# Optimization experiments

Hardware: AMD Instinct MI355X
Metric: run time of the kernel (lower is better)

Reference implementation:

```python
import jax, jax.numpy as jnp
import numpy as np

B, H, L, C = 16, 512, 4096, 1
LAM = 0.001  # kernel squash threshold (lam in LongConvKernel)


def setup_inputs() -> dict:
    key = jax.random.key(0)
    ks = jax.random.split(key, 5)
    u = jax.random.normal(ks[0], (B, H, L), jnp.float32)
    # LongConvKernel 'double_exp' init: K ~ N(0, 0.02^2) * exp(-(j/L) * (H//2)^(i/H))
    K = jax.random.normal(ks[1], (C, H, L), jnp.float32) * 0.02
    i = jnp.arange(H, dtype=jnp.float32)[:, None]
    j = jnp.arange(L, dtype=jnp.float32)[None, :]
    double_exp = jnp.exp(-(j / L) * jnp.power(float(H // 2), i / H))  # (H, L)
    kernel = K * double_exp[None]
    D = jax.random.normal(ks[2], (C, H), jnp.float32)  # skip connection params
    # TransposedLinear(C*H -> H): weight (d_output, d_input), kaiming-ish scale
    Wout = jax.random.normal(ks[3], (H, C * H), jnp.float32) / np.sqrt(C * H)
    bout = jax.random.normal(ks[4], (H,), jnp.float32) * 0.01
    return {"u": u, "kernel": kernel, "D": D, "Wout": Wout, "bout": bout}


def reference(u, kernel, D, Wout, bout):
    Lseq = u.shape[-1]
    # kernel squashing: relu(|k| - lam) * sign(k)  (soft-threshold)
    k = jax.nn.relu(jnp.abs(kernel) - LAM) * jnp.sign(kernel)  # (C, H, L)
    n = 2 * Lseq
    k_f = jnp.fft.rfft(k, n=n, axis=-1)            # (C, H, n//2+1) complex
    u_f = jnp.fft.rfft(u, n=n, axis=-1)            # (B, H, n//2+1) complex
    y_f = jnp.einsum('bhl,chl->bchl', u_f, k_f)    # pointwise multiply in freq
    y = jnp.fft.irfft(y_f, n=n, axis=-1)[..., :Lseq]  # (B, C, H, L)
    y = y + jnp.einsum('bhl,ch->bchl', u, D)       # skip term
    y = y.reshape(y.shape[0], C * H, Lseq)         # (B, C*H, L)
    y = jax.nn.gelu(y, approximate=False)          # activation (torch GELU = exact)
    # output_linear: TransposedLinear + swish postact
    y = jnp.einsum('bul,vu->bvl', y, Wout) + bout[None, :, None]
    y = jax.nn.silu(y)
    return y
```

## Files before the change

### kernel.cpp

```cpp
#include <hip/hip_runtime.h>
#include <hip/hip_bf16.h>
#include <math.h>

#define BB 16
#define HH 512
#define LL 4096
#define NFFT 8192
#define LAM 0.001f

typedef __attribute__((ext_vector_type(8))) short short8;
typedef __attribute__((ext_vector_type(4))) float floatx4;

#define R2C 0.70710678118654752f

__device__ __forceinline__ void cmul(float ar, float ai, float br, float bi,
                                     float& cr, float& ci) {
  cr = ar * br - ai * bi;
  ci = ar * bi + ai * br;
}

constexpr float W16C[8] = {1.f, 0.92387953f, 0.70710678f, 0.38268343f, 0.f,
                           -0.38268343f, -0.70710678f, -0.92387953f};
constexpr float W16S[8] = {0.f, -0.38268343f, -0.70710678f, -0.92387953f, -1.f,
                           -0.92387953f, -0.70710678f, -0.38268343f};
constexpr int BR8[8] = {0, 4, 2, 6, 1, 5, 3, 7};
constexpr float W16CB[8] = {W16C[0], W16C[4], W16C[2], W16C[6],
                            W16C[1], W16C[5], W16C[3], W16C[7]};
constexpr float W16SB[8] = {W16S[0], W16S[4], W16S[2], W16S[6],
                            W16S[1], W16S[5], W16S[3], W16S[7]};

__device__ __forceinline__ int slotf(int a) { return a ^ ((a >> 4) & 15); }

__device__ __forceinline__ void fft8(float* r, float* i) {
  float t0r = r[0] + r[4], t0i = i[0] + i[4], u0r = r[0] - r[4], u0i = i[0] - i[4];
  float t1r = r[1] + r[5], t1i = i[1] + i[5], u1r = r[1] - r[5], u1i = i[1] - i[5];
  float t2r = r[2] + r[6], t2i = i[2] + i[6], u2r = r[2] - r[6], u2i = i[2] - i[6];
  float t3r = r[3] + r[7], t3i = i[3] + i[7], u3r = r[3] - r[7], u3i = i[3] - i[7];
  float w1r = R2C * (u1r + u1i), w1i = R2C * (u1i - u1r);
  float w2r = u2i, w2i = -u2r;
  float w3r = R2C * (u3i - u3r), w3i = -R2C * (u3r + u3i);
  float p0r = t0r + t2r, p0i = t0i + t2i, q0r = t0r - t2r, q0i = t0i - t2i;
  float p1r = t1r + t3r, p1i = t1i + t3i, q1r = t1r - t3r, q1i = t1i - t3i;
  float s1r = q1i, s1i = -q1r;
  float v0r = u0r + w2r, v0i = u0i + w2i, x0r = u0r - w2r, x0i = u0i - w2i;
  float v1r = w1r + w3r, v1i = w1i + w3i, x1r = w1r - w3r, x1i = w1i - w3i;
  float y1r = x1i, y1i = -x1r;
  r[0] = p0r + p1r; i[0] = p0i + p1i;
  r[1] = p0r - p1r; i[1] = p0i - p1i;
  r[2] = q0r + s1r; i[2] = q0i + s1i;
  r[3] = q0r - s1r; i[3] = q0i - s1i;
  r[4] = v0r + v1r; i[4] = v0i + v1i;
  r[5] = v0r - v1r; i[5] = v0i - v1i;
  r[6] = x0r + y1r; i[6] = x0i + y1i;
  r[7] = x0r - y1r; i[7] = x0i - y1i;
}

__device__ __forceinline__ void fft8_pad4(float* r, float* i) {
  float x0r = r[0], x0i = i[0], x1r = r[1], x1i = i[1];
  float x2r = r[2], x2i = i[2], x3r = r[3], x3i = i[3];
  float w1r = R2C * (x1r + x1i), w1i = R2C * (x1i - x1r);
  float w2r = x2i, w2i = -x2r;
  float w3r = R2C * (x3i - x3r), w3i = -R2C * (x3r + x3i);
  float p0r = x0r + x2r, p0i = x0i + x2i, q0r = x0r - x2r, q0i = x0i - x2i;
  float p1r = x1r + x3r, p1i = x1i + x3i, q1r = x1r - x3r, q1i = x1i - x3i;
  float s1r = q1i, s1i = -q1r;
  float v0r = x0r + w2r, v0i = x0i + w2i, m0r = x0r - w2r, m0i = x0i - w2i;
  float v1r = w1r + w3r, v1i = w1i + w3i, m1r = w1r - w3r, m1i = w1i - w3i;
  float y1r = m1i, y1i = -m1r;
  r[0] = p0r + p1r; i[0] = p0i + p1i;
  r[1] = p0r - p1r; i[1] = p0i - p1i;
  r[2] = q0r + s1r; i[2] = q0i + s1i;
  r[3] = q0r - s1r; i[3] = q0i - s1i;
  r[4] = v0r + v1r; i[4] = v0i + v1i;
  r[5] = v0r - v1r; i[5] = v0i - v1i;
  r[6] = m0r + y1r; i[6] = m0i + y1i;
  r[7] = m0r - y1r; i[7] = m0i - y1i;
}

__device__ __forceinline__ void ifft8(float* r, float* i) {
  float p0r = r[0] + r[1], p0i = i[0] + i[1];
  float p1r = r[0] - r[1], p1i = i[0] - i[1];
  float q0r = r[2] + r[3], q0i = i[2] + i[3];
  float s1r = r[2] - r[3], s1i = i[2] - i[3];
  float v0r = r[4] + r[5], v0i = i[4] + i[5];
  float v1r = r[4] - r[5], v1i = i[4] - i[5];
  float x0r = r[6] + r[7], x0i = i[6] + i[7];
  float y1r = r[6] - r[7], y1i = i[6] - i[7];
  float q1r = -s1i, q1i = s1r;
  float x1r = -y1i, x1i = y1r;
  float t0r = p0r + q0r, t0i = p0i + q0i, t2r = p0r - q0r, t2i = p0i - q0i;
  float t1r = p1r + q1r, t1i = p1i + q1i, t3r = p1r - q1r, t3i = p1i - q1i;
  float a0r = v0r + x0r, a0i = v0i + x0i, a2r = v0r - x0r, a2i = v0i - x0i;
  float a1r = v1r + x1r, a1i = v1i + x1i, a3r = v1r - x1r, a3i = v1i - x1i;
  float u1r = R2C * (a1r - a1i), u1i = R2C * (a1r + a1i);
  float u2r = -a2i, u2i = a2r;
  float u3r = -R2C * (a3r + a3i), u3i = R2C * (a3r - a3i);
  r[0] = t0r + a0r; i[0] = t0i + a0i;  r[4] = t0r - a0r; i[4] = t0i - a0i;
  r[1] = t1r + u1r; i[1] = t1i + u1i;  r[5] = t1r - u1r; i[5] = t1i - u1i;
  r[2] = t2r + u2r; i[2] = t2i + u2i;  r[6] = t2r - u2r; i[6] = t2i - u2i;
  r[3] = t3r + u3r; i[3] = t3i + u3i;  r[7] = t3r - u3r; i[7] = t3i - u3i;
}

__device__ __forceinline__ void ifft8_head4(float* r, float* i) {
  float p0r = r[0] + r[1], p0i = i[0] + i[1];
  float p1r = r[0] - r[1], p1i = i[0] - i[1];
  float q0r = r[2] + r[3], q0i = i[2] + i[3];
  float s1r = r[2] - r[3], s1i = i[2] - i[3];
  float v0r = r[4] + r[5], v0i = i[4] + i[5];
  float v1r = r[4] - r[5], v1i = i[4] - i[5];
  float x0r = r[6] + r[7], x0i = i[6] + i[7];
  float y1r = r[6] - r[7], y1i = i[6] - i[7];
  float q1r = -s1i, q1i = s1r;
  float x1r = -y1i, x1i = y1r;
  float t0r = p0r + q0r, t0i = p0i + q0i, t2r = p0r - q0r, t2i = p0i - q0i;
  float t1r = p1r + q1r, t1i = p1i + q1i, t3r = p1r - q1r, t3i = p1i - q1i;
  float a0r = v0r + x0r, a0i = v0i + x0i, a2r = v0r - x0r, a2i = v0i - x0i;
  float a1r = v1r + x1r, a1i = v1i + x1i, a3r = v1r - x1r, a3i = v1i - x1i;
  float u1r = R2C * (a1r - a1i), u1i = R2C * (a1r + a1i);
  float u2r = -a2i, u2i = a2r;
  float u3r = -R2C * (a3r + a3i), u3i = R2C * (a3r - a3i);
  r[0] = t0r + a0r; i[0] = t0i + a0i;
  r[1] = t1r + u1r; i[1] = t1i + u1i;
  r[2] = t2r + u2r; i[2] = t2i + u2i;
  r[3] = t3r + u3r; i[3] = t3i + u3i;
}

__device__ __forceinline__ float gelu_exact(float y) {
  return 0.5f * y * (1.f + erff(y * 0.70710678118654752f));
}

template <int LOGJ>
__device__ __forceinline__ void r8_fwd(float2* sb, int t, const float4* tw) {
  const int J = 1 << LOGJ;
  const int j = t & (J - 1);
  const int base = (t >> LOGJ) << (LOGJ + 3);
  float xr[8], xi[8];
#pragma unroll
  for (int s = 0; s < 8; ++s) {
    float2 v = sb[slotf(base + j + (s << LOGJ))];
    xr[s] = v.x; xi[s] = v.y;
  }
  fft8(xr, xi);
#pragma unroll
  for (int q = 0; q < 4; ++q) {
    float4 w = tw[(q << LOGJ) + j];
    float tr, ti;
    cmul(xr[2 * q], xi[2 * q], w.x, w.y, tr, ti);
    sb[slotf(base + (BR8[2 * q] << LOGJ) + j)] = make_float2(tr, ti);
    cmul(xr[2 * q + 1], xi[2 * q + 1], w.z, w.w, tr, ti);
    sb[slotf(base + (BR8[2 * q + 1] << LOGJ) + j)] = make_float2(tr, ti);
  }
}

template <int LOGJ>
__device__ __forceinline__ void r8_inv(float2* sb, int t, const float4* tw) {
  const int J = 1 << LOGJ;
  const int j = t & (J - 1);
  const int base = (t >> LOGJ) << (LOGJ + 3);
  float xr[8], xi[8];
#pragma unroll
  for (int q = 0; q < 4; ++q) {
    float4 w = tw[(q << LOGJ) + j];
    float2 v0 = sb[slotf(base + (BR8[2 * q] << LOGJ) + j)];
    cmul(v0.x, v0.y, w.x, -w.y, xr[2 * q], xi[2 * q]);
    float2 v1 = sb[slotf(base + (BR8[2 * q + 1] << LOGJ) + j)];
    cmul(v1.x, v1.y, w.z, -w.w, xr[2 * q + 1], xi[2 * q + 1]);
  }
  ifft8(xr, xi);
#pragma unroll
  for (int s = 0; s < 8; ++s)
    sb[slotf(base + j + (s << LOGJ))] = make_float2(xr[s], xi[s]);
}

__device__ __forceinline__ void p1_scatter(float2* sb, int j, const float4* tw1,
                                           float* xr, float* xi) {
#pragma unroll
  for (int q = 0; q < 4; ++q) {
    float4 w = tw1[(q << 10) + j];
    float tr, ti;
    cmul(xr[2 * q], xi[2 * q], w.x, w.y, tr, ti);
    sb[slotf((BR8[2 * q] << 10) + j)] = make_float2(tr, ti);
    cmul(xr[2 * q + 1], xi[2 * q + 1], w.z, w.w, tr, ti);
    sb[slotf((BR8[2 * q + 1] << 10) + j)] = make_float2(tr, ti);
  }
}

__device__ __forceinline__ void p4_bins(float2* sb, int t, float* br_, float* bi_) {
  const int p = t >> 1, par = t & 1;
  const int a0 = (p << 4) + par;
  float xr[8], xi[8];
#pragma unroll
  for (int e = 0; e < 8; ++e) {
    float2 v = sb[slotf(a0 + 2 * e)];
    xr[e] = v.x; xi[e] = v.y;
  }
  fft8(xr, xi);
#pragma unroll
  for (int s = 0; s < 8; ++s) {
    float tr, ti;
    if (par) { cmul(xr[s], xi[s], W16CB[s], W16SB[s], tr, ti); }
    else { tr = xr[s]; ti = xi[s]; }
    float orr = __shfl_xor(tr, 1);
    float oii = __shfl_xor(ti, 1);
    br_[s] = par ? (orr - tr) : (tr + orr);
    bi_[s] = par ? (oii - ti) : (ti + oii);
  }
}

__device__ __forceinline__ void p4_inv(float2* sb, int t, float* br_, float* bi_) {
  const int p = t >> 1, par = t & 1;
  const int a0 = (p << 4) + par;
  float yr[8], yi[8];
#pragma unroll
  for (int s = 0; s < 8; ++s) {
    float orr = __shfl_xor(br_[s], 1);
    float oii = __shfl_xor(bi_[s], 1);
    float er = par ? (orr - br_[s]) : (br_[s] + orr);
    float ei = par ? (oii - bi_[s]) : (bi_[s] + oii);
    if (par) { float tr, ti; cmul(er, ei, W16CB[s], -W16SB[s], tr, ti); er = tr; ei = ti; }
    yr[s] = er; yi[s] = ei;
  }
  ifft8(yr, yi);
#pragma unroll
  for (int e = 0; e < 8; ++e)
    sb[slotf(a0 + 2 * e)] = make_float2(yr[e], yi[e]);
}

__global__ __launch_bounds__(1024) void twgen_kernel(float4* __restrict__ tw1,
                                                     float4* __restrict__ tw2,
                                                     float4* __restrict__ tw3) {
  const int j = threadIdx.x;
#pragma unroll
  for (int q = 0; q < 4; ++q) {
    const int m0 = BR8[2 * q], m1 = BR8[2 * q + 1];
    float s0, c0, s1, c1;
    const float a1 = -6.283185307179586f / 8192.f;
    sincosf(a1 * (float)(j * m0), &s0, &c0);
    sincosf(a1 * (float)(j * m1), &s1, &c1);
    tw1[(q << 10) + j] = make_float4(c0, s0, c1, s1);
    if (j < 128) {
      const float a2 = -6.283185307179586f / 1024.f;
      sincosf(a2 * (float)(j * m0), &s0, &c0);
      sincosf(a2 * (float)(j * m1), &s1, &c1);
      tw2[(q << 7) + j] = make_float4(c0, s0, c1, s1);
    }
    if (j < 16) {
      const float a3 = -6.283185307179586f / 128.f;
      sincosf(a3 * (float)(j * m0), &s0, &c0);
      sincosf(a3 * (float)(j * m1), &s1, &c1);
      tw3[(q << 4) + j] = make_float4(c0, s0, c1, s1);
    }
  }
}

__global__ void wconv_kernel(const float* __restrict__ W,
                             __hip_bfloat16* __restrict__ Wb) {
  int i = blockIdx.x * 256 + threadIdx.x;
  Wb[i] = __float2bfloat16(W[i]);
}

__global__ __launch_bounds__(1024)
void kf_kernel(const float* __restrict__ kern, const float* __restrict__ D,
               float* __restrict__ Kf, const float4* __restrict__ tw1,
               const float4* __restrict__ tw2, const float4* __restrict__ tw3) {
  __shared__ __align__(16) float2 sb[NFFT];
  __shared__ __align__(16) float4 ltw2[512];
  __shared__ __align__(16) float4 ltw3[64];
  const int t = threadIdx.x;
  const int h = blockIdx.x;
  const float* kr = kern + (size_t)h * LL;
  if (t < 512) ltw2[t] = tw2[t];
  if (t < 64) ltw3[t] = tw3[t];
  {
    float xr[8], xi[8];
#pragma unroll
    for (int s = 0; s < 4; ++s) {
      float kv = kr[t + (s << 10)];
      float a = fabsf(kv) - LAM;
      float sq = (a > 0.f) ? ((kv > 0.f) ? a : -a) : 0.f;
      xr[s] = sq * (1.f / 8192.f);
      xi[s] = 0.f;
    }
    fft8_pad4(xr, xi);
    p1_scatter(sb, t, tw1, xr, xi);
  }
  __syncthreads();
  r8_fwd<7>(sb, t, ltw2);
  __syncthreads();
  r8_fwd<4>(sb, t, ltw3);
  {
    float br_[8], bi_[8];
    p4_bins(sb, t, br_, bi_);
    const float dsc = D[h] * (1.f / 8192.f);
    float4* out4 = (float4*)(Kf + (size_t)h * NFFT * 2) + (t << 2);
#pragma unroll
    for (int q = 0; q < 4; ++q)
      out4[q] = make_float4(br_[2 * q] + dsc, bi_[2 * q],
                            br_[2 * q + 1] + dsc, bi_[2 * q + 1]);
  }
}

__global__ __launch_bounds__(1024)
void fftconv_kernel(const float* __restrict__ u, const float* __restrict__ Kf,
                    __hip_bfloat16* __restrict__ g, const float4* __restrict__ tw1,
                    const float4* __restrict__ tw2, const float4* __restrict__ tw3) {
  __shared__ __align__(16) float2 sb[NFFT];
  __shared__ __align__(16) float4 ltw2[512];
  __shared__ __align__(16) float4 ltw3[64];
  const int t = threadIdx.x;
  const int h = blockIdx.x;
  const int p = blockIdx.y;
  const int b0 = 2 * p, b1 = 2 * p + 1;
  const float* u0 = u + ((size_t)(b0 * HH + h)) * LL;
  const float* u1 = u + ((size_t)(b1 * HH + h)) * LL;

  if (t < 512) ltw2[t] = tw2[t];
  if (t < 64) ltw3[t] = tw3[t];

  {
    float xr[8], xi[8];
#pragma unroll
    for (int s = 0; s < 4; ++s) {
      xr[s] = u0[t + (s << 10)];
      xi[s] = u1[t + (s << 10)];
    }
    fft8_pad4(xr, xi);
    p1_scatter(sb, t, tw1, xr, xi);
  }
  __syncthreads();
  r8_fwd<7>(sb, t, ltw2);
  __syncthreads();
  r8_fwd<4>(sb, t, ltw3);
  {
    float br_[8], bi_[8];
    p4_bins(sb, t, br_, bi_);
    const float4* kf4 = (const float4*)(Kf + (size_t)h * NFFT * 2) + (t << 2);
#pragma unroll
    for (int q = 0; q < 4; ++q) {
      float4 kk = kf4[q];
      float tr, ti;
      cmul(br_[2 * q], bi_[2 * q], kk.x, kk.y, tr, ti);
      br_[2 * q] = tr; bi_[2 * q] = ti;
      cmul(br_[2 * q + 1], bi_[2 * q + 1], kk.z, kk.w, tr, ti);
      br_[2 * q + 1] = tr; bi_[2 * q + 1] = ti;
    }
    p4_inv(sb, t, br_, bi_);
  }
  r8_inv<4>(sb, t, ltw3);
  __syncthreads();
  r8_inv<7>(sb, t, ltw2);
  __syncthreads();
  {
    float xr[8], xi[8];
#pragma unroll
    for (int q = 0; q < 4; ++q) {
      float4 w = tw1[(q << 10) + t];
      float2 v0 = sb[slotf((BR8[2 * q] << 10) + t)];
      cmul(v0.x, v0.y, w.x, -w.y, xr[2 * q], xi[2 * q]);
      float2 v1 = sb[slotf((BR8[2 * q + 1] << 10) + t)];
      cmul(v1.x, v1.y, w.z, -w.w, xr[2 * q + 1], xi[2 * q + 1]);
    }
    ifft8_head4(xr, xi);
    __hip_bfloat16* g0 = g + ((size_t)(b0 * HH + h)) * LL;
    __hip_bfloat16* g1 = g + ((size_t)(b1 * HH + h)) * LL;
#pragma unroll
    for (int s = 0; s < 4; ++s) {
      g0[t + (s << 10)] = __float2bfloat16(gelu_exact(xr[s]));
      g1[t + (s << 10)] = __float2bfloat16(gelu_exact(xi[s]));
    }
  }
}

__global__ __launch_bounds__(256) void transpose_kernel(
    const __hip_bfloat16* __restrict__ g, __hip_bfloat16* __restrict__ g2) {
  __shared__ unsigned short tile[64][72];
  const int lb = blockIdx.x;
  const int hb = blockIdx.y;
  const int b = blockIdx.z;
  const int l0 = lb * 64, h0 = hb * 64;
  const int tid = threadIdx.x;
  const int r = tid >> 3;
  const int gc = tid & 7;
  const int c = gc * 8;
  const unsigned short* gs = (const unsigned short*)g;
  unsigned short* g2s = (unsigned short*)g2;
  for (int it = 0; it < 2; ++it) {
    int rr = r + it * 32;
    int4 v = *(const int4*)(gs + ((size_t)(b * HH + h0 + rr)) * LL + l0 + c);
    *(int4*)&tile[rr][(gc ^ (rr >> 3)) << 3] = v;
  }
  __syncthreads();
  for (int it = 0; it < 2; ++it) {
    int rr = r + it * 32;
    const int pc = (rr & 7) | (((rr >> 3) ^ gc) << 3);
    unsigned short vals[8];
#pragma unroll
    for (int j = 0; j < 8; ++j) vals[j] = tile[c + j][pc];
    *(int4*)(g2s + ((size_t)(b * LL + l0 + rr)) * HH + h0 + c) = *(int4*)vals;
  }
}

__global__ __launch_bounds__(256, 4) void gemm_kernel(
    const __hip_bfloat16* __restrict__ Wb, const __hip_bfloat16* __restrict__ g2,
    const float* __restrict__ bout, float* __restrict__ out) {
  const int vt = blockIdx.x;
  const int lt = blockIdx.y;
  const int b = blockIdx.z;
  const int wave = threadIdx.x >> 6;
  const int ln = threadIdx.x & 63;
  const int wr = wave >> 1, wc = wave & 1;
  const int vbase = vt * 128 + wr * 64;
  const int lbase = lt * 128 + wc * 64;
  const int lane16 = ln & 15;
  const int quad = ln >> 4;

  floatx4 acc[4][4];
#pragma unroll
  for (int mi = 0; mi < 4; ++mi)
#pragma unroll
    for (int ni = 0; ni < 4; ++ni) acc[mi][ni] = (floatx4){0.f, 0.f, 0.f, 0.f};

  const unsigned short* A = (const unsigned short*)Wb;
  const unsigned short* Bm = (const unsigned short*)g2 + (size_t)b * LL * HH;

  for (int k0 = 0; k0 < HH; k0 += 32) {
    const int kk = k0 + quad * 8;
    short8 af[4], bf[4];
#pragma unroll
    for (int mi = 0; mi < 4; ++mi) {
      const int m = vbase + mi * 16 + lane16;
      af[mi] = *(const short8*)(A + (size_t)m * HH + kk);
    }
#pragma unroll
    for (int ni = 0; ni < 4; ++ni) {
      const int n = lbase + ni * 16 + lane16;
      bf[ni] = *(const short8*)(Bm + (size_t)n * HH + kk);
    }
#pragma unroll
    for (int mi = 0; mi < 4; ++mi)
#pragma unroll
      for (int ni = 0; ni < 4; ++ni)
        acc[mi][ni] = __builtin_amdgcn_mfma_f32_16x16x32_bf16(af[mi], bf[ni],
                                                              acc[mi][ni], 0, 0, 0);
  }

#pragma unroll
  for (int mi = 0; mi < 4; ++mi) {
#pragma unroll
    for (int r = 0; r < 4; ++r) {
      const int m = vbase + mi * 16 + quad * 4 + r;
      const float bias = bout[m];
#pragma unroll
      for (int ni = 0; ni < 4; ++ni) {
        const int n = lbase + ni * 16 + lane16;
        float y = acc[mi][ni][r] + bias;
        y = y / (1.f + __expf(-y));
        out[((size_t)(b * HH + m)) * LL + n] = y;
      }
    }
  }
}

extern "C" void kernel_launch(void* const* d_in, const int* in_sizes, int n_in,
                              void* d_out, int out_size, void* d_ws, size_t ws_size,
                              hipStream_t stream) {
  const float* u = (const float*)d_in[0];
  const float* kern = (const float*)d_in[1];
  const float* D = (const float*)d_in[2];
  const float* Wout = (const float*)d_in[3];
  const float* bout = (const float*)d_in[4];
  float* out = (float*)d_out;

  char* ws = (char*)d_ws;
  const size_t KF_BYTES = (size_t)HH * NFFT * sizeof(float2);
  const size_t G_BYTES = (size_t)BB * HH * LL * 2;
  float* Kf = (float*)ws;
  __hip_bfloat16* g = (__hip_bfloat16*)(ws + KF_BYTES);
  __hip_bfloat16* g2 = (__hip_bfloat16*)(ws + KF_BYTES + G_BYTES);
  __hip_bfloat16* Wb = (__hip_bfloat16*)(ws + KF_BYTES + 2 * G_BYTES);
  float4* tw1 = (float4*)g2;
  float4* tw2 = tw1 + 4 * 1024;
  float4* tw3 = tw2 + 4 * 128;

  twgen_kernel<<<dim3(1), dim3(1024), 0, stream>>>(tw1, tw2, tw3);
  wconv_kernel<<<dim3((HH * HH) / 256), dim3(256), 0, stream>>>(Wout, Wb);
  kf_kernel<<<dim3(HH), dim3(1024), 0, stream>>>(kern, D, Kf, tw1, tw2, tw3);
  fftconv_kernel<<<dim3(HH, BB / 2), dim3(1024), 0, stream>>>(u, Kf, g, tw1, tw2, tw3);
  transpose_kernel<<<dim3(LL / 64, HH / 64, BB), dim3(256), 0, stream>>>(g, g2);
  gemm_kernel<<<dim3(HH / 128, LL / 128, BB), dim3(256), 0, stream>>>(Wb, g2, bout, out);
}
```

Baseline: 537.8 us.

## Fuse transpose into GEMM via double-buffered LDS staging of activations

```diff
diff --git a/kernel.cpp b/kernel.cpp
--- a/kernel.cpp
+++ b/kernel.cpp
@@ -371,46 +371,22 @@
   }
 }
 
-__global__ __launch_bounds__(256) void transpose_kernel(
-    const __hip_bfloat16* __restrict__ g, __hip_bfloat16* __restrict__ g2) {
-  __shared__ unsigned short tile[64][72];
-  const int lb = blockIdx.x;
-  const int hb = blockIdx.y;
-  const int b = blockIdx.z;
-  const int l0 = lb * 64, h0 = hb * 64;
+#define BKP 40
+__global__ __launch_bounds__(256, 4) void gemm_kernel(
+    const __hip_bfloat16* __restrict__ Wb, const __hip_bfloat16* __restrict__ g,
+    const float* __restrict__ bout, float* __restrict__ out) {
+  __shared__ unsigned short bt[2][128][BKP];
+  const int id = blockIdx.x;
+  const int w = (id & 7) * 256 + (id >> 3);
+  const int vt = w & 3;
+  const int lt = (w >> 2) & 31;
+  const int b = w >> 7;
   const int tid = threadIdx.x;
-  const int r = tid >> 3;
-  const int gc = tid & 7;
-  const int c = gc * 8;
-  const unsigned short* gs = (const unsigned short*)g;
-  unsigned short* g2s = (unsigned short*)g2;
-  for (int it = 0; it < 2; ++it) {
-    int rr = r + it * 32;
-    int4 v = *(const int4*)(gs + ((size_t)(b * HH + h0 + rr)) * LL + l0 + c);
-    *(int4*)&tile[rr][(gc ^ (rr >> 3)) << 3] = v;
-  }
-  __syncthreads();
-  for (int it = 0; it < 2; ++it) {
-    int rr = r + it * 32;
-    const int pc = (rr & 7) | (((rr >> 3) ^ gc) << 3);
-    unsigned short vals[8];
-#pragma unroll
-    for (int j = 0; j < 8; ++j) vals[j] = tile[c + j][pc];
-    *(int4*)(g2s + ((size_t)(b * LL + l0 + rr)) * HH + h0 + c) = *(int4*)vals;
-  }
-}
-
-__global__ __launch_bounds__(256, 4) void gemm_kernel(
-    const __hip_bfloat16* __restrict__ Wb, const __hip_bfloat16* __restrict__ g2,
-    const float* __restrict__ bout, float* __restrict__ out) {
-  const int vt = blockIdx.x;
-  const int lt = blockIdx.y;
-  const int b = blockIdx.z;
-  const int wave = threadIdx.x >> 6;
-  const int ln = threadIdx.x & 63;
+  const int wave = tid >> 6;
+  const int ln = tid & 63;
   const int wr = wave >> 1, wc = wave & 1;
   const int vbase = vt * 128 + wr * 64;
-  const int lbase = lt * 128 + wc * 64;
+  const int lbase0 = lt * 128;
   const int lane16 = ln & 15;
   const int quad = ln >> 4;
 
@@ -421,20 +397,38 @@
     for (int ni = 0; ni < 4; ++ni) acc[mi][ni] = (floatx4){0.f, 0.f, 0.f, 0.f};
 
   const unsigned short* A = (const unsigned short*)Wb;
-  const unsigned short* Bm = (const unsigned short*)g2 + (size_t)b * LL * HH;
-
-  for (int k0 = 0; k0 < HH; k0 += 32) {
-    const int kk = k0 + quad * 8;
+  const unsigned short* gb = (const unsigned short*)g + (size_t)b * HH * LL;
+
+#define STAGE_B(BUF, K0)                                                       \
+  {                                                                            \
+    _Pragma("unroll") for (int it = 0; it < 2; ++it) {                         \
+      const int uu = tid + it * 256;                                           \
+      const int ho = uu >> 4;                                                  \
+      const int lo = (uu & 15) * 8;                                            \
+      int4 v = *(const int4*)(gb + (size_t)((K0) + ho) * LL + lbase0 + lo);    \
+      unsigned short vs[8];                                                    \
+      *(int4*)vs = v;                                                          \
+      _Pragma("unroll") for (int e = 0; e < 8; ++e) bt[BUF][lo + e][ho] = vs[e]; \
+    }                                                                          \
+  }
+
+  STAGE_B(0, 0);
+  __syncthreads();
+
+  for (int s = 0; s < 16; ++s) {
+    const int cur = s & 1;
+    if (s < 15) STAGE_B(cur ^ 1, (s + 1) * 32);
+    const int kk = quad * 8;
     short8 af[4], bf[4];
 #pragma unroll
     for (int mi = 0; mi < 4; ++mi) {
       const int m = vbase + mi * 16 + lane16;
-      af[mi] = *(const short8*)(A + (size_t)m * HH + kk);
+      af[mi] = *(const short8*)(A + (size_t)m * HH + s * 32 + kk);
     }
 #pragma unroll
     for (int ni = 0; ni < 4; ++ni) {
-      const int n = lbase + ni * 16 + lane16;
-      bf[ni] = *(const short8*)(Bm + (size_t)n * HH + kk);
+      const int nloc = wc * 64 + ni * 16 + lane16;
+      bf[ni] = *(const short8*)(&bt[cur][nloc][kk]);
     }
 #pragma unroll
     for (int mi = 0; mi < 4; ++mi)
@@ -442,6 +436,7 @@
       for (int ni = 0; ni < 4; ++ni)
         acc[mi][ni] = __builtin_amdgcn_mfma_f32_16x16x32_bf16(af[mi], bf[ni],
                                                               acc[mi][ni], 0, 0, 0);
+    __syncthreads();
   }
 
 #pragma unroll
@@ -452,13 +447,14 @@
       const float bias = bout[m];
 #pragma unroll
       for (int ni = 0; ni < 4; ++ni) {
-        const int n = lbase + ni * 16 + lane16;
+        const int n = lbase0 + wc * 64 + ni * 16 + lane16;
         float y = acc[mi][ni][r] + bias;
         y = y / (1.f + __expf(-y));
         out[((size_t)(b * HH + m)) * LL + n] = y;
       }
     }
   }
+#undef STAGE_B
 }
 
 extern "C" void kernel_launch(void* const* d_in, const int* in_sizes, int n_in,
@@ -476,9 +472,8 @@
   const size_t G_BYTES = (size_t)BB * HH * LL * 2;
   float* Kf = (float*)ws;
   __hip_bfloat16* g = (__hip_bfloat16*)(ws + KF_BYTES);
-  __hip_bfloat16* g2 = (__hip_bfloat16*)(ws + KF_BYTES + G_BYTES);
   __hip_bfloat16* Wb = (__hip_bfloat16*)(ws + KF_BYTES + 2 * G_BYTES);
-  float4* tw1 = (float4*)g2;
+  float4* tw1 = (float4*)(ws + KF_BYTES + G_BYTES);
   float4* tw2 = tw1 + 4 * 1024;
   float4* tw3 = tw2 + 4 * 128;
 
@@ -486,6 +481,5 @@
   wconv_kernel<<<dim3((HH * HH) / 256), dim3(256), 0, stream>>>(Wout, Wb);
   kf_kernel<<<dim3(HH), dim3(1024), 0, stream>>>(kern, D, Kf, tw1, tw2, tw3);
   fftconv_kernel<<<dim3(HH, BB / 2), dim3(1024), 0, stream>>>(u, Kf, g, tw1, tw2, tw3);
-  transpose_kernel<<<dim3(LL / 64, HH / 64, BB), dim3(256), 0, stream>>>(g, g2);
-  gemm_kernel<<<dim3(HH / 128, LL / 128, BB), dim3(256), 0, stream>>>(Wb, g2, bout, out);
-}
+  gemm_kernel<<<dim3(2048), dim3(256), 0, stream>>>(Wb, g, bout, out);
+}
```

Result: no change. 531.4 us (-1.2%).
